# Performance work log

Measured on AMD Instinct MI355X. Metric: run time of the kernel, lower is better.

The kernel has to match this reference:

```python
import jax, jax.numpy as jnp
import numpy as np

N_NODES = 100000
N_EDGES = 800000
D_IN, D_H1, D_H2, D_OUT = 512, 256, 256, 64


def setup_inputs() -> dict:
    key = jax.random.key(0)
    ks = jax.random.split(key, 8)
    x = jax.random.normal(ks[0], (N_NODES, D_IN), dtype=jnp.float32)
    edge_index = jax.random.randint(ks[1], (2, N_EDGES), 0, N_NODES, dtype=jnp.int64)
    # Glorot-style scaled weights (PyG GCNConv uses glorot init; Linear uses kaiming-uniform).
    W1 = jax.random.normal(ks[2], (D_IN, D_H1), dtype=jnp.float32) / np.sqrt(D_IN)
    b1 = jnp.zeros((D_H1,), dtype=jnp.float32)
    W2 = jax.random.normal(ks[3], (D_H1, D_H2), dtype=jnp.float32) / np.sqrt(D_H1)
    b2 = jnp.zeros((D_H2,), dtype=jnp.float32)
    Wc = jax.random.normal(ks[4], (D_H2, D_OUT), dtype=jnp.float32) / np.sqrt(D_H2)
    bc = jnp.zeros((D_OUT,), dtype=jnp.float32)
    return {"x": x, "edge_index": edge_index, "W1": W1, "b1": b1,
            "W2": W2, "b2": b2, "Wc": Wc, "bc": bc}


def reference(x, edge_index, W1, b1, W2, b2, Wc, bc):
    # GCNModel.forward in eval mode (dropout is identity when training=False).
    N = x.shape[0]
    src, dst = edge_index[0], edge_index[1]
    # PyG GCNConv: add self-loops, symmetric normalization D^-1/2 (A+I) D^-1/2.
    deg = jnp.zeros((N,), x.dtype).at[dst].add(jnp.float32(1.0)) + 1.0  # in-degree + self-loop
    dinv = jax.lax.rsqrt(deg)                         # [N]
    norm = dinv[src] * dinv[dst]                      # [E] per-edge coefficient
    self_norm = (dinv * dinv)[:, None]                # [N,1] self-loop coefficient 1/deg

    def gcn_conv(h, W, b):
        h = h @ W                                     # transform first (PyG order)
        agg = jax.ops.segment_sum(h[src] * norm[:, None], dst, num_segments=N)
        return agg + h * self_norm + b

    h = jax.nn.relu(gcn_conv(x, W1, b1))
    h = jax.nn.relu(gcn_conv(h, W2, b2))
    return h @ Wc + bc                                # [N, num_classes]
```

## Files before the change

### kernel.cpp

```cpp
#include <hip/hip_runtime.h>
#include <cstdint>

#define DIN 512
#define DH  256
#define DOUT 64

typedef __attribute__((ext_vector_type(8))) short bf16x8;
typedef __attribute__((ext_vector_type(4))) float f32x4;
typedef unsigned int uint32;

__device__ __forceinline__ unsigned short f2bf(float f) {
    uint32 u = __float_as_uint(f);
    u += 0x7fff + ((u >> 16) & 1);
    return (unsigned short)(u >> 16);
}
__device__ __forceinline__ float bflo(uint32 u) { return __uint_as_float(u << 16); }
__device__ __forceinline__ float bfhi(uint32 u) { return __uint_as_float(u & 0xffff0000u); }
__device__ __forceinline__ uint32 pk2(float lo, float hi) {
    return (uint32)f2bf(lo) | ((uint32)f2bf(hi) << 16);
}

__global__ void detect_i64(const unsigned long long* ei, int n_check,
                           unsigned long long bound, int* flag) {
    __shared__ int ok;
    if (threadIdx.x == 0) ok = 1;
    __syncthreads();
    int bad = 0;
    for (int i = threadIdx.x; i < n_check; i += blockDim.x) {
        if (ei[i] >= bound) bad = 1;
    }
    if (bad) ok = 0;
    __syncthreads();
    if (threadIdx.x == 0) *flag = ok;
}

__device__ __forceinline__ int get_idx(const void* ei, int is64, int pos) {
    if (is64) return (int)((const long long*)ei)[pos];
    return ((const int*)ei)[pos];
}

__global__ void count_deg(const void* ei, const int* flag, int E, int* counts) {
    const int is64 = *flag;
    int e = blockIdx.x * blockDim.x + threadIdx.x;
    if (e >= E) return;
    int d = get_idx(ei, is64, E + e);
    atomicAdd(&counts[d], 1);
}

__global__ void compute_dinv(const int* counts, float* dinv, int N) {
    int i = blockIdx.x * blockDim.x + threadIdx.x;
    if (i < N) dinv[i] = rsqrtf((float)counts[i] + 1.0f);
}

#define SCAN_BLOCK 256
#define SCAN_ELEMS 1024

__global__ void scan1(const int* counts, int* out, int* blocksums, int N) {
    __shared__ int sh[SCAN_BLOCK];
    int base = blockIdx.x * SCAN_ELEMS;
    int t = threadIdx.x;
    int v[4];
    int s = 0;
    #pragma unroll
    for (int j = 0; j < 4; j++) {
        int idx = base + t * 4 + j;
        v[j] = (idx < N) ? counts[idx] : 0;
        s += v[j];
    }
    sh[t] = s;
    __syncthreads();
    for (int off = 1; off < SCAN_BLOCK; off <<= 1) {
        int x = (t >= off) ? sh[t - off] : 0;
        __syncthreads();
        sh[t] += x;
        __syncthreads();
    }
    int run = (t == 0) ? 0 : sh[t - 1];
    #pragma unroll
    for (int j = 0; j < 4; j++) {
        int idx = base + t * 4 + j;
        if (idx < N) out[idx] = run;
        run += v[j];
    }
    if (t == SCAN_BLOCK - 1) blocksums[blockIdx.x] = sh[t];
}

__global__ void scan2(int* blocksums, int NB) {
    __shared__ int sh[SCAN_BLOCK];
    int t = threadIdx.x;
    sh[t] = (t < NB) ? blocksums[t] : 0;
    __syncthreads();
    for (int off = 1; off < SCAN_BLOCK; off <<= 1) {
        int x = (t >= off) ? sh[t - off] : 0;
        __syncthreads();
        sh[t] += x;
        __syncthreads();
    }
    if (t < NB) blocksums[t] = (t == 0) ? 0 : sh[t - 1];
}

__global__ void scan3(int* row_ptr, const int* blocksums, int N, int E) {
    int i = blockIdx.x * blockDim.x + threadIdx.x;
    if (i < N) row_ptr[i] += blocksums[i / SCAN_ELEMS];
    if (i == N) row_ptr[N] = E;
}

__global__ void fill_csr(const void* ei, const int* flag, int E,
                         const int* row_ptr, int* cursor, int2* edges,
                         const float* dinv) {
    const int is64 = *flag;
    int e = blockIdx.x * blockDim.x + threadIdx.x;
    if (e >= E) return;
    int d = get_idx(ei, is64, E + e);
    int s = get_idx(ei, is64, e);
    int pos = row_ptr[d] + atomicAdd(&cursor[d], 1);
    edges[pos] = make_int2(s, __float_as_int(dinv[s] * dinv[d]));
}

__global__ void transpose_w(const float* __restrict__ W, unsigned short* __restrict__ Bt,
                            int K, int Nw) {
    int i = blockIdx.x * blockDim.x + threadIdx.x;
    if (i >= K * Nw) return;
    int k = i / Nw, n = i % Nw;
    Bt[(size_t)n * K + k] = f2bf(W[i]);
}

__global__ __launch_bounds__(256) void gemm1_mfma(const float* __restrict__ Af,
                                                  const unsigned short* __restrict__ Bt,
                                                  unsigned short* __restrict__ C,
                                                  int M, int K) {
    __shared__ unsigned short lds[16384];
    unsigned short* As = lds;
    const int tid = threadIdx.x;
    const int w = tid >> 6, l = tid & 63;
    const int m0 = blockIdx.x * 64;

    f32x4 acc[4][4] = {};

    for (int k0 = 0; k0 < K; k0 += 64) {
        __syncthreads();
        #pragma unroll
        for (int i = 0; i < 2; i++) {
            int row = i * 32 + (tid >> 3);
            int g = tid & 7;
            int rg = m0 + row; if (rg > M - 1) rg = M - 1;
            const float* s = Af + (size_t)rg * K + k0 + g * 8;
            float4 v0 = *(const float4*)s;
            float4 v1 = *(const float4*)(s + 4);
            uint4 o;
            o.x = pk2(v0.x, v0.y); o.y = pk2(v0.z, v0.w);
            o.z = pk2(v1.x, v1.y); o.w = pk2(v1.z, v1.w);
            *(uint4*)(As + row * 64 + ((g ^ (row & 7)) * 8)) = o;
        }
        __syncthreads();
        #pragma unroll
        for (int ks = 0; ks < 2; ks++) {
            bf16x8 a[4], b[4];
            #pragma unroll
            for (int m = 0; m < 4; m++) {
                int ar = m * 16 + (l & 15);
                int q = (ks * 4 + (l >> 4)) ^ (ar & 7);
                a[m] = *(const bf16x8*)(As + ar * 64 + q * 8);
            }
            #pragma unroll
            for (int n = 0; n < 4; n++) {
                int br = w * 64 + n * 16 + (l & 15);
                b[n] = *(const bf16x8*)(Bt + (size_t)br * K + k0 + ks * 32 + (l >> 4) * 8);
            }
            #pragma unroll
            for (int m = 0; m < 4; m++)
                #pragma unroll
                for (int n = 0; n < 4; n++)
                    acc[m][n] = __builtin_amdgcn_mfma_f32_16x16x32_bf16(a[m], b[n], acc[m][n], 0, 0, 0);
        }
    }
    __syncthreads();
    unsigned short* ep = lds + w * 4096;
    #pragma unroll
    for (int m = 0; m < 4; m++)
        #pragma unroll
        for (int n = 0; n < 4; n++)
            #pragma unroll
            for (int r = 0; r < 4; r++)
                ep[(m * 16 + (l >> 4) * 4 + r) * 64 + n * 16 + (l & 15)] = f2bf(acc[m][n][r]);
    __syncthreads();
    #pragma unroll
    for (int p = 0; p < 8; p++) {
        int row = p * 8 + (l >> 3);
        int gr = m0 + row;
        uint4 v = *(const uint4*)(ep + row * 64 + (l & 7) * 8);
        if (gr < M)
            *(uint4*)(C + (size_t)gr * 256 + w * 64 + (l & 7) * 8) = v;
    }
}

__global__ __launch_bounds__(512) void gemm2_persist(const unsigned short* __restrict__ A,
                                                     const unsigned short* __restrict__ Bt,
                                                     unsigned short* __restrict__ C,
                                                     int M) {
    __shared__ unsigned short lds[73728];
    unsigned short* Bs = lds;
    unsigned short* As = lds + 65536;
    const int tid = threadIdx.x;
    const int w = tid >> 6, l = tid & 63;
    const int wr = w >> 2, wc = w & 3;

    #pragma unroll
    for (int i = 0; i < 16; i++) {
        int gi = i * 512 + tid;
        int r = gi >> 5, g = gi & 31;
        int gs = g ^ (r & 7);
        __builtin_amdgcn_global_load_lds(
            (const __attribute__((address_space(1))) uint32*)(Bt + (size_t)r * 256 + gs * 8),
            (__attribute__((address_space(3))) uint32*)(Bs + (size_t)gi * 8), 16, 0, 0);
    }

    const int sr = tid >> 3;
    const int sg = tid & 7;

    for (int mt = blockIdx.x; mt * 64 < M; mt += gridDim.x) {
        const int m0 = mt * 64;
        {
            int rg = m0 + sr; if (rg > M - 1) rg = M - 1;
            int gq = sg ^ (sr & 7);
            __builtin_amdgcn_global_load_lds(
                (const __attribute__((address_space(1))) uint32*)(A + (size_t)rg * 256 + gq * 8),
                (__attribute__((address_space(3))) uint32*)(As + tid * 8), 16, 0, 0);
        }
        __syncthreads();

        f32x4 acc[2][4] = {};
        #pragma unroll
        for (int k = 0; k < 4; k++) {
            if (k < 3) {
                int rg = m0 + sr; if (rg > M - 1) rg = M - 1;
                int gq = sg ^ (sr & 7);
                __builtin_amdgcn_global_load_lds(
                    (const __attribute__((address_space(1))) uint32*)(A + (size_t)rg * 256 + (k + 1) * 64 + gq * 8),
                    (__attribute__((address_space(3))) uint32*)(As + ((k + 1) & 1) * 4096 + tid * 8), 16, 0, 0);
            }
            const unsigned short* Ab = As + (k & 1) * 4096;
            #pragma unroll
            for (int ks = 0; ks < 2; ks++) {
                bf16x8 a[2], b[4];
                #pragma unroll
                for (int m = 0; m < 2; m++) {
                    int ar = wr * 32 + m * 16 + (l & 15);
                    int q = (ks * 4 + (l >> 4)) ^ (ar & 7);
                    a[m] = *(const bf16x8*)(Ab + ar * 64 + q * 8);
                }
                #pragma unroll
                for (int n = 0; n < 4; n++) {
                    int br = wc * 64 + n * 16 + (l & 15);
                    int gabs = k * 8 + ks * 4 + (l >> 4);
                    int q = gabs ^ (br & 7);
                    b[n] = *(const bf16x8*)(Bs + br * 256 + q * 8);
                }
                #pragma unroll
                for (int m = 0; m < 2; m++)
                    #pragma unroll
                    for (int n = 0; n < 4; n++)
                        acc[m][n] = __builtin_amdgcn_mfma_f32_16x16x32_bf16(a[m], b[n], acc[m][n], 0, 0, 0);
            }
            __syncthreads();
        }

        #pragma unroll
        for (int m = 0; m < 2; m++)
            #pragma unroll
            for (int r = 0; r < 4; r++) {
                int row = m0 + wr * 32 + m * 16 + (l >> 4) * 4 + r;
                if (row >= M) continue;
                #pragma unroll
                for (int n = 0; n < 4; n++) {
                    int col = wc * 64 + n * 16 + (l & 15);
                    C[(size_t)row * 256 + col] = f2bf(acc[m][n][r]);
                }
            }
    }
}

__global__ __launch_bounds__(256) void gemm_head(const unsigned short* __restrict__ A,
                                                 const unsigned short* __restrict__ Bt,
                                                 const float* __restrict__ bias,
                                                 float* __restrict__ out, int M) {
    __shared__ unsigned short As[128 * 64];
    __shared__ unsigned short Bs[64 * 64];
    const int tid = threadIdx.x;
    const int w = tid >> 6, l = tid & 63;
    const int m0 = blockIdx.x * 128;
    const int wr = w >> 1, wc = w & 1;
    f32x4 acc[4][2] = {};

    for (int k0 = 0; k0 < 256; k0 += 64) {
        #pragma unroll
        for (int i = 0; i < 4; i++) {
            int row = i * 32 + (tid >> 3);
            int gq = (tid & 7) ^ (row & 7);
            int rg = m0 + row; if (rg > M - 1) rg = M - 1;
            __builtin_amdgcn_global_load_lds(
                (const __attribute__((address_space(1))) uint32*)(A + (size_t)rg * 256 + k0 + gq * 8),
                (__attribute__((address_space(3))) uint32*)(As + row * 64 + (tid & 7) * 8), 16, 0, 0);
        }
        #pragma unroll
        for (int i = 0; i < 2; i++) {
            int row = i * 32 + (tid >> 3);
            int gq = (tid & 7) ^ (row & 7);
            __builtin_amdgcn_global_load_lds(
                (const __attribute__((address_space(1))) uint32*)(Bt + (size_t)row * 256 + k0 + gq * 8),
                (__attribute__((address_space(3))) uint32*)(Bs + row * 64 + (tid & 7) * 8), 16, 0, 0);
        }
        __syncthreads();
        #pragma unroll
        for (int ks = 0; ks < 2; ks++) {
            bf16x8 a[4], b[2];
            #pragma unroll
            for (int m = 0; m < 4; m++) {
                int arow = wr * 64 + m * 16 + (l & 15);
                int ag = (ks * 4 + (l >> 4)) ^ (arow & 7);
                a[m] = *(const bf16x8*)(As + arow * 64 + ag * 8);
            }
            #pragma unroll
            for (int n = 0; n < 2; n++) {
                int brow = wc * 32 + n * 16 + (l & 15);
                int bg = (ks * 4 + (l >> 4)) ^ (brow & 7);
                b[n] = *(const bf16x8*)(Bs + brow * 64 + bg * 8);
            }
            #pragma unroll
            for (int m = 0; m < 4; m++)
                #pragma unroll
                for (int n = 0; n < 2; n++)
                    acc[m][n] = __builtin_amdgcn_mfma_f32_16x16x32_bf16(a[m], b[n], acc[m][n], 0, 0, 0);
        }
        __syncthreads();
    }
    #pragma unroll
    for (int m = 0; m < 4; m++)
        #pragma unroll
        for (int n = 0; n < 2; n++)
            #pragma unroll
            for (int r = 0; r < 4; r++) {
                int gr = m0 + wr * 64 + m * 16 + (l >> 4) * 4 + r;
                int col = wc * 32 + n * 16 + (l & 15);
                if (gr < M) out[(size_t)gr * 64 + col] = acc[m][n][r] + bias[col];
            }
}

#define ACC8(v, wgt)                                    \
    do {                                                \
        acc[0] = fmaf(wgt, bflo(v.x), acc[0]);          \
        acc[1] = fmaf(wgt, bfhi(v.x), acc[1]);          \
        acc[2] = fmaf(wgt, bflo(v.y), acc[2]);          \
        acc[3] = fmaf(wgt, bfhi(v.y), acc[3]);          \
        acc[4] = fmaf(wgt, bflo(v.z), acc[4]);          \
        acc[5] = fmaf(wgt, bfhi(v.z), acc[5]);          \
        acc[6] = fmaf(wgt, bflo(v.w), acc[6]);          \
        acc[7] = fmaf(wgt, bfhi(v.w), acc[7]);          \
    } while (0)

__global__ __launch_bounds__(256) void aggregate_bf(const unsigned short* __restrict__ t,
                                                    const float* __restrict__ dinv,
                                                    const int* __restrict__ row_ptr,
                                                    const int2* __restrict__ edges,
                                                    const float* __restrict__ bias,
                                                    unsigned short* __restrict__ outb,
                                                    int N) {
    int wave = threadIdx.x >> 6;
    int lane = threadIdx.x & 63;
    int half = lane >> 5;
    int sl = lane & 31;
    int n = blockIdx.x * 8 + wave * 2 + half;
    if (n >= N) return;

    float dn = dinv[n];
    int r0 = row_ptr[n], r1 = row_ptr[n + 1];

    float acc[8];
    {
        uint4 sv = *(const uint4*)(t + (size_t)n * DH + sl * 8);
        float sn = dn * dn;
        acc[0] = bflo(sv.x) * sn; acc[1] = bfhi(sv.x) * sn;
        acc[2] = bflo(sv.y) * sn; acc[3] = bfhi(sv.y) * sn;
        acc[4] = bflo(sv.z) * sn; acc[5] = bfhi(sv.z) * sn;
        acc[6] = bflo(sv.w) * sn; acc[7] = bfhi(sv.w) * sn;
    }

    int j = r0;
    for (; j + 4 <= r1; j += 4) {
        int2 e0 = edges[j + 0], e1 = edges[j + 1];
        int2 e2 = edges[j + 2], e3 = edges[j + 3];
        uint4 v0 = *(const uint4*)(t + (size_t)e0.x * DH + sl * 8);
        uint4 v1 = *(const uint4*)(t + (size_t)e1.x * DH + sl * 8);
        uint4 v2 = *(const uint4*)(t + (size_t)e2.x * DH + sl * 8);
        uint4 v3 = *(const uint4*)(t + (size_t)e3.x * DH + sl * 8);
        float w0 = __int_as_float(e0.y), w1 = __int_as_float(e1.y);
        float w2 = __int_as_float(e2.y), w3 = __int_as_float(e3.y);
        ACC8(v0, w0); ACC8(v1, w1); ACC8(v2, w2); ACC8(v3, w3);
    }
    for (; j < r1; j++) {
        int2 e = edges[j];
        float wgt = __int_as_float(e.y);
        uint4 v = *(const uint4*)(t + (size_t)e.x * DH + sl * 8);
        ACC8(v, wgt);
    }

    float4 b0 = *(const float4*)(bias + sl * 8);
    float4 b1v = *(const float4*)(bias + sl * 8 + 4);
    acc[0] = fmaxf(acc[0] + b0.x, 0.f);  acc[1] = fmaxf(acc[1] + b0.y, 0.f);
    acc[2] = fmaxf(acc[2] + b0.z, 0.f);  acc[3] = fmaxf(acc[3] + b0.w, 0.f);
    acc[4] = fmaxf(acc[4] + b1v.x, 0.f); acc[5] = fmaxf(acc[5] + b1v.y, 0.f);
    acc[6] = fmaxf(acc[6] + b1v.z, 0.f); acc[7] = fmaxf(acc[7] + b1v.w, 0.f);

    uint4 o;
    o.x = pk2(acc[0], acc[1]);
    o.y = pk2(acc[2], acc[3]);
    o.z = pk2(acc[4], acc[5]);
    o.w = pk2(acc[6], acc[7]);
    *(uint4*)(outb + (size_t)n * DH + sl * 8) = o;
}

extern "C" void kernel_launch(void* const* d_in, const int* in_sizes, int n_in,
                              void* d_out, int out_size, void* d_ws, size_t ws_size,
                              hipStream_t stream) {
    const float* x  = (const float*)d_in[0];
    const void*  ei = d_in[1];
    const float* W1 = (const float*)d_in[2];
    const float* b1 = (const float*)d_in[3];
    const float* W2 = (const float*)d_in[4];
    const float* b2 = (const float*)d_in[5];
    const float* Wc = (const float*)d_in[6];
    const float* bc = (const float*)d_in[7];
    float* out = (float*)d_out;

    const int N = in_sizes[0] / DIN;
    const int E = in_sizes[1] / 2;

    char* ws = (char*)d_ws;
    size_t off = 0;
    auto alloc = [&](size_t bytes) -> void* {
        off = (off + 255) & ~(size_t)255;
        void* p = ws + off;
        off += bytes;
        return p;
    };

    int*   flag      = (int*)alloc(4);
    int*   counts    = (int*)alloc((size_t)N * 4);
    int*   cursor    = (int*)alloc((size_t)N * 4);
    int*   row_ptr   = (int*)alloc((size_t)(N + 1) * 4);
    int2*  edges     = (int2*)alloc((size_t)E * 8);
    int*   blocksums = (int*)alloc(1024 * 4);
    float* dinv      = (float*)alloc((size_t)N * 4);
    unsigned short* Bt1   = (unsigned short*)alloc((size_t)DH * DIN * 2);
    unsigned short* Bt2   = (unsigned short*)alloc((size_t)DH * DH * 2);
    unsigned short* Btc   = (unsigned short*)alloc((size_t)DOUT * DH * 2);
    unsigned short* t_buf = (unsigned short*)alloc((size_t)N * DH * 2);
    unsigned short* a_buf = (unsigned short*)alloc((size_t)N * DH * 2);

    const int NB = (N + SCAN_ELEMS - 1) / SCAN_ELEMS;
    const int gM64  = (N + 63) / 64;
    const int gM128 = (N + 127) / 128;

    detect_i64<<<1, 256, 0, stream>>>((const unsigned long long*)ei, 1024,
                                      (unsigned long long)N, flag);
    transpose_w<<<(DIN * DH + 255) / 256, 256, 0, stream>>>(W1, Bt1, DIN, DH);
    transpose_w<<<(DH * DH + 255) / 256, 256, 0, stream>>>(W2, Bt2, DH, DH);
    transpose_w<<<(DH * DOUT + 255) / 256, 256, 0, stream>>>(Wc, Btc, DH, DOUT);

    hipMemsetAsync(counts, 0, (size_t)N * 8 + 256, stream);
    count_deg<<<(E + 255) / 256, 256, 0, stream>>>(ei, flag, E, counts);
    compute_dinv<<<(N + 255) / 256, 256, 0, stream>>>(counts, dinv, N);
    scan1<<<NB, SCAN_BLOCK, 0, stream>>>(counts, row_ptr, blocksums, N);
    scan2<<<1, SCAN_BLOCK, 0, stream>>>(blocksums, NB);
    scan3<<<(N + 1 + 255) / 256, 256, 0, stream>>>(row_ptr, blocksums, N, E);
    fill_csr<<<(E + 255) / 256, 256, 0, stream>>>(ei, flag, E, row_ptr, cursor, edges, dinv);

    gemm1_mfma<<<gM64, 256, 0, stream>>>(x, Bt1, t_buf, N, DIN);
    aggregate_bf<<<(N + 7) / 8, 256, 0, stream>>>(t_buf, dinv, row_ptr, edges, b1, a_buf, N);
    gemm2_persist<<<256, 512, 0, stream>>>(a_buf, Bt2, t_buf, N);
    aggregate_bf<<<(N + 7) / 8, 256, 0, stream>>>(t_buf, dinv, row_ptr, edges, b2, a_buf, N);
    gemm_head<<<gM128, 256, 0, stream>>>(a_buf, Btc, bc, out, N);
}
```

Before: 383.1 us.

## Retile first GEMM into 128x128 blocks with B staged in LDS

The first-layer GEMM changes from 64-row by 256-column tiles into 128x128 tiles. The grid now splits the output columns across two blocks. B (the transposed W1) is now copied into swizzled LDS with direct global-to-LDS loads, instead of each wave reading its fragments straight from global memory. This should cut repeated global B traffic and raise per-wave MFMA reuse. In exchange, every fp32 row of x is now read by two blocks, which relies on L2 to avoid doubling the traffic on the dominant input. A bf16-input template variant is also added but is not used.

```diff
diff --git a/kernel.cpp b/kernel.cpp
--- a/kernel.cpp
+++ b/kernel.cpp
@@ -125,32 +125,59 @@
     Bt[(size_t)n * K + k] = f2bf(W[i]);
 }
 
-__global__ __launch_bounds__(256) void gemm1_mfma(const float* __restrict__ Af,
-                                                  const unsigned short* __restrict__ Bt,
-                                                  unsigned short* __restrict__ C,
-                                                  int M, int K) {
+template <bool A_FP32>
+__global__ __launch_bounds__(256) void gemm_mfma(const void* __restrict__ Ap,
+                                                 const unsigned short* __restrict__ Bt,
+                                                 unsigned short* __restrict__ C,
+                                                 int M, int K) {
     __shared__ unsigned short lds[16384];
     unsigned short* As = lds;
+    unsigned short* Bs = lds + 8192;
     const int tid = threadIdx.x;
     const int w = tid >> 6, l = tid & 63;
-    const int m0 = blockIdx.x * 64;
+    const int m0 = (blockIdx.x >> 1) * 128;
+    const int n0 = (blockIdx.x & 1) * 128;
+    const int wr = w >> 1, wc = w & 1;
 
     f32x4 acc[4][4] = {};
 
     for (int k0 = 0; k0 < K; k0 += 64) {
-        __syncthreads();
-        #pragma unroll
-        for (int i = 0; i < 2; i++) {
-            int row = i * 32 + (tid >> 3);
-            int g = tid & 7;
-            int rg = m0 + row; if (rg > M - 1) rg = M - 1;
-            const float* s = Af + (size_t)rg * K + k0 + g * 8;
-            float4 v0 = *(const float4*)s;
-            float4 v1 = *(const float4*)(s + 4);
-            uint4 o;
-            o.x = pk2(v0.x, v0.y); o.y = pk2(v0.z, v0.w);
-            o.z = pk2(v1.x, v1.y); o.w = pk2(v1.z, v1.w);
-            *(uint4*)(As + row * 64 + ((g ^ (row & 7)) * 8)) = o;
+        #pragma unroll
+        for (int i = 0; i < 4; i++) {
+            int gi = i * 256 + tid;
+            int row = gi >> 3, g = gi & 7;
+            int gs = g ^ (row & 7);
+            __builtin_amdgcn_global_load_lds(
+                (const __attribute__((address_space(1))) uint32*)(Bt + (size_t)(n0 + row) * K + k0 + gs * 8),
+                (__attribute__((address_space(3))) uint32*)(Bs + row * 64 + g * 8), 16, 0, 0);
+        }
+        if (A_FP32) {
+            const float* Af = (const float*)Ap;
+            #pragma unroll
+            for (int i = 0; i < 4; i++) {
+                int gi = i * 256 + tid;
+                int row = gi >> 3, g = gi & 7;
+                int rg = m0 + row; if (rg > M - 1) rg = M - 1;
+                const float* s = Af + (size_t)rg * K + k0 + g * 8;
+                float4 v0 = *(const float4*)s;
+                float4 v1 = *(const float4*)(s + 4);
+                uint4 o;
+                o.x = pk2(v0.x, v0.y); o.y = pk2(v0.z, v0.w);
+                o.z = pk2(v1.x, v1.y); o.w = pk2(v1.z, v1.w);
+                *(uint4*)(As + row * 64 + ((g ^ (row & 7)) * 8)) = o;
+            }
+        } else {
+            const unsigned short* Ab = (const unsigned short*)Ap;
+            #pragma unroll
+            for (int i = 0; i < 4; i++) {
+                int gi = i * 256 + tid;
+                int row = gi >> 3, g = gi & 7;
+                int gs = g ^ (row & 7);
+                int rg = m0 + row; if (rg > M - 1) rg = M - 1;
+                __builtin_amdgcn_global_load_lds(
+                    (const __attribute__((address_space(1))) uint32*)(Ab + (size_t)rg * K + k0 + gs * 8),
+                    (__attribute__((address_space(3))) uint32*)(As + row * 64 + g * 8), 16, 0, 0);
+            }
         }
         __syncthreads();
         #pragma unroll
@@ -158,14 +185,15 @@
             bf16x8 a[4], b[4];
             #pragma unroll
             for (int m = 0; m < 4; m++) {
-                int ar = m * 16 + (l & 15);
+                int ar = wr * 64 + m * 16 + (l & 15);
                 int q = (ks * 4 + (l >> 4)) ^ (ar & 7);
                 a[m] = *(const bf16x8*)(As + ar * 64 + q * 8);
             }
             #pragma unroll
             for (int n = 0; n < 4; n++) {
-                int br = w * 64 + n * 16 + (l & 15);
-                b[n] = *(const bf16x8*)(Bt + (size_t)br * K + k0 + ks * 32 + (l >> 4) * 8);
+                int br = wc * 64 + n * 16 + (l & 15);
+                int q = (ks * 4 + (l >> 4)) ^ (br & 7);
+                b[n] = *(const bf16x8*)(Bs + br * 64 + q * 8);
             }
             #pragma unroll
             for (int m = 0; m < 4; m++)
@@ -173,8 +201,9 @@
                 for (int n = 0; n < 4; n++)
                     acc[m][n] = __builtin_amdgcn_mfma_f32_16x16x32_bf16(a[m], b[n], acc[m][n], 0, 0, 0);
         }
-    }
-    __syncthreads();
+        __syncthreads();
+    }
+
     unsigned short* ep = lds + w * 4096;
     #pragma unroll
     for (int m = 0; m < 4; m++)
@@ -187,10 +216,10 @@
     #pragma unroll
     for (int p = 0; p < 8; p++) {
         int row = p * 8 + (l >> 3);
-        int gr = m0 + row;
+        int gr = m0 + wr * 64 + row;
         uint4 v = *(const uint4*)(ep + row * 64 + (l & 7) * 8);
         if (gr < M)
-            *(uint4*)(C + (size_t)gr * 256 + w * 64 + (l & 7) * 8) = v;
+            *(uint4*)(C + (size_t)gr * 256 + n0 + wc * 64 + (l & 7) * 8) = v;
     }
 }
 
@@ -458,7 +487,6 @@
     unsigned short* a_buf = (unsigned short*)alloc((size_t)N * DH * 2);
 
     const int NB = (N + SCAN_ELEMS - 1) / SCAN_ELEMS;
-    const int gM64  = (N + 63) / 64;
     const int gM128 = (N + 127) / 128;
 
     detect_i64<<<1, 256, 0, stream>>>((const unsigned long long*)ei, 1024,
@@ -475,7 +503,7 @@
     scan3<<<(N + 1 + 255) / 256, 256, 0, stream>>>(row_ptr, blocksums, N, E);
     fill_csr<<<(E + 255) / 256, 256, 0, stream>>>(ei, flag, E, row_ptr, cursor, edges, dinv);
 
-    gemm1_mfma<<<gM64, 256, 0, stream>>>(x, Bt1, t_buf, N, DIN);
+    gemm_mfma<true><<<2 * gM128, 256, 0, stream>>>(x, Bt1, t_buf, N, DIN);
     aggregate_bf<<<(N + 7) / 8, 256, 0, stream>>>(t_buf, dinv, row_ptr, edges, b1, a_buf, N);
     gemm2_persist<<<256, 512, 0, stream>>>(a_buf, Bt2, t_buf, N);
     aggregate_bf<<<(N + 7) / 8, 256, 0, stream>>>(t_buf, dinv, row_ptr, edges, b2, a_buf, N);
```

Measured after the change: 368.1 us. -3.9%, faster.
